# Performance work log

Measured on AMD Instinct MI355X. Metric: run time of the kernel, lower is better.

The kernel has to match this reference:

```python
import jax, jax.numpy as jnp
import numpy as np

N_NODES = 20000
N_EDGES = 320000
IN_F = 256
OUT_F = 64
HEADS = 4
ALPHA = 0.1  # leaky_relu negative slope


def setup_inputs() -> dict:
    key = jax.random.key(0)
    ks = jax.random.split(key, 8)
    return {
        "input1": jax.random.normal(ks[0], (N_NODES, IN_F), jnp.float32),
        "input2": jax.random.normal(ks[1], (N_NODES, IN_F), jnp.float32),
        # per-head params: Ws maps source feats -> target_out, Wt maps target feats -> source_out
        "Ws": jax.random.normal(ks[2], (HEADS, IN_F, OUT_F), jnp.float32) * 0.06,
        "Wt": jax.random.normal(ks[3], (HEADS, IN_F, OUT_F), jnp.float32) * 0.06,
        "a1": jax.random.normal(ks[4], (HEADS, 2 * OUT_F), jnp.float32) * 0.1,
        "a2": jax.random.normal(ks[5], (HEADS, 2 * OUT_F), jnp.float32) * 0.1,
        # COO nonzeros of A_opt [n_target, n_source]
        "tgt_idx": jax.random.randint(ks[6], (N_EDGES,), 0, N_NODES),
        "src_idx": jax.random.randint(ks[7], (N_EDGES,), 0, N_NODES),
    }


def _segment_softmax(scores, seg, num_segments):
    m = jax.lax.stop_gradient(jax.ops.segment_max(scores, seg, num_segments=num_segments))
    w = jnp.exp(scores - m[seg])
    d = jax.ops.segment_sum(w, seg, num_segments=num_segments)
    d = jnp.where(d == 0, 1.0, d)
    return w / d[seg]


def _head(x1, x2, Ws, Wt, a1, a2, src, tgt, n_s, n_t):
    s = x1 @ Ws  # [n_s, OUT_F]  messages source -> target
    t = x2 @ Wt  # [n_t, OUT_F]  messages target -> source
    out = Ws.shape[1]
    # edge score e = leaky_relu(a^T [s_src || t_tgt]); split a to avoid edge-level concat
    e1 = jax.nn.leaky_relu((s @ a1[:out])[src] + (t @ a1[out:])[tgt], ALPHA)
    e2 = jax.nn.leaky_relu((s @ a2[:out])[src] + (t @ a2[out:])[tgt], ALPHA)
    alpha_ts = _segment_softmax(e1, tgt, n_t)  # softmax over sources per target
    alpha_st = _segment_softmax(e2, src, n_s)  # softmax over targets per source
    h_ts = jax.ops.segment_sum(alpha_ts[:, None] * s[src], tgt, num_segments=n_t)
    h_st = jax.ops.segment_sum(alpha_st[:, None] * t[tgt], src, num_segments=n_s)
    return jax.nn.elu(h_st), jax.nn.elu(h_ts)  # concat=True -> ELU per head


def reference(input1, input2, Ws, Wt, a1, a2, tgt_idx, src_idx):
    n_s, n_t = input1.shape[0], input2.shape[0]
    head_fn = jax.vmap(
        lambda W1, W2, v1, v2: _head(input1, input2, W1, W2, v1, v2, src_idx, tgt_idx, n_s, n_t)
    )
    h_st, h_ts = head_fn(Ws, Wt, a1, a2)  # each [H, n, OUT_F]
    h_st = jnp.transpose(h_st, (1, 0, 2)).reshape(n_s, -1)  # concat heads
    h_ts = jnp.transpose(h_ts, (1, 0, 2)).reshape(n_t, -1)
    return h_st, h_ts
```

## Files before the change

### kernel.cpp

```cpp
#include <hip/hip_runtime.h>
#include <math.h>

#define N_NODES 20000
#define N_EDGES 320000
#define IN_F 256
#define OUT_F 64
#define HEADS 4
#define NCOL 256
#define LRELU_ALPHA 0.1f
#define ELL_CAP 64

typedef __attribute__((ext_vector_type(8))) short short8;
typedef __attribute__((ext_vector_type(4))) float floatx4;

__device__ __forceinline__ float lrelu(float x) {
    return x > 0.f ? x : LRELU_ALPHA * x;
}
__device__ __forceinline__ unsigned short f2bf(float f) {
    unsigned int u = __float_as_uint(f);
    u = (u + 0x7FFF + ((u >> 16) & 1)) >> 16;
    return (unsigned short)u;
}
__device__ __forceinline__ float bf2f(unsigned short u) {
    return __uint_as_float(((unsigned int)u) << 16);
}

__global__ __launch_bounds__(256) void prep_build_kernel(
    const int* __restrict__ src, const int* __restrict__ tgt,
    const float* __restrict__ Ws, const float* __restrict__ Wt,
    unsigned short* __restrict__ Wsb, unsigned short* __restrict__ Wtb,
    int* __restrict__ cnt_t, int* __restrict__ cnt_s,
    int* __restrict__ elist_t, int* __restrict__ elist_s)
{
    const int tid = threadIdx.x;
    if (blockIdx.x < 64) {
        const int gid = blockIdx.x * 256 + tid;
        const int mat = gid >> 13;
        const int r   = gid & 8191;
        const int kc  = r >> 8;
        const int c   = r & 255;
        const float* W    = mat ? Wt : Ws;
        unsigned short* O = mat ? Wtb : Wsb;
        const int h = c >> 6, j = c & 63;
        const int k0 = kc * 8;
        unsigned short v[8] __attribute__((aligned(16)));
#pragma unroll
        for (int i = 0; i < 8; ++i)
            v[i] = f2bf(W[(size_t)h * (IN_F * OUT_F) + (size_t)(k0 + i) * OUT_F + j]);
        *(uint4*)(O + (size_t)c * IN_F + k0) = *(const uint4*)v;
    } else {
        const int e = (blockIdx.x - 64) * 256 + tid;
        if (e < N_EDGES) {
            int sn = src[e], tn = tgt[e];
            int p = atomicAdd(&cnt_t[tn], 1);
            if (p < ELL_CAP) elist_t[tn * ELL_CAP + p] = sn;
            int q = atomicAdd(&cnt_s[sn], 1);
            if (q < ELL_CAP) elist_s[sn * ELL_CAP + q] = tn;
        }
    }
}

__global__ __launch_bounds__(256) void gemm_mfma_kernel(
    const float* __restrict__ A0, const unsigned short* __restrict__ Wb0,
    const float* __restrict__ A1, const unsigned short* __restrict__ Wb1,
    unsigned short* __restrict__ C0, unsigned short* __restrict__ C1,
    const float* __restrict__ a1, const float* __restrict__ a2,
    float* __restrict__ ss1, float* __restrict__ ss2,
    float* __restrict__ tt1, float* __restrict__ tt2)
{
    const float* A           = (blockIdx.y == 0) ? A0 : A1;
    const unsigned short* Wb = (blockIdx.y == 0) ? Wb0 : Wb1;
    unsigned short* C        = (blockIdx.y == 0) ? C0 : C1;

    __shared__ __align__(16) unsigned short Bl[256][40];

    const int tid   = threadIdx.x;
    const int lane  = tid & 63;
    const int w     = tid >> 6;
    const int quad  = lane >> 4;
    const int l15   = lane & 15;
    const int mhalf = w & 1, nhalf = w >> 1;
    const int r0    = blockIdx.x * 32;
    const int mrow  = r0 + mhalf * 16 + l15;

    floatx4 acc[8];
#pragma unroll
    for (int t = 0; t < 8; ++t) acc[t] = (floatx4){0.f, 0.f, 0.f, 0.f};

    const float* arow = A + (size_t)mrow * IN_F + quad * 8;

    for (int k0 = 0; k0 < IN_F; k0 += 32) {
#pragma unroll
        for (int p = 0; p < 4; ++p) {
            int idx = p * 256 + tid;
            int n = idx >> 2, kc = idx & 3;
            uint4 v = *(const uint4*)(Wb + (size_t)n * 256 + k0 + kc * 8);
            *(uint4*)&Bl[n][kc * 8] = v;
        }
        __syncthreads();

        float4 av0 = *(const float4*)(arow + k0);
        float4 av1 = *(const float4*)(arow + k0 + 4);
        short8 afrag;
        afrag[0] = (short)f2bf(av0.x); afrag[1] = (short)f2bf(av0.y);
        afrag[2] = (short)f2bf(av0.z); afrag[3] = (short)f2bf(av0.w);
        afrag[4] = (short)f2bf(av1.x); afrag[5] = (short)f2bf(av1.y);
        afrag[6] = (short)f2bf(av1.z); afrag[7] = (short)f2bf(av1.w);

#pragma unroll
        for (int t = 0; t < 8; ++t) {
            int n = (nhalf * 8 + t) * 16 + l15;
            short8 bfrag = *(const short8*)&Bl[n][quad * 8];
            acc[t] = __builtin_amdgcn_mfma_f32_16x16x32_bf16(afrag, bfrag, acc[t], 0, 0, 0);
        }
        __syncthreads();
    }

#pragma unroll
    for (int t = 0; t < 8; ++t) {
        int col = (nhalf * 8 + t) * 16 + l15;
#pragma unroll
        for (int r = 0; r < 4; ++r) {
            int m = r0 + mhalf * 16 + quad * 4 + r;
            C[(size_t)m * NCOL + col] = f2bf(acc[t][r]);
        }
    }

    const int off_aj = (blockIdx.y == 0) ? 0 : 64;
    float* o1 = (blockIdx.y == 0) ? ss1 : tt1;
    float* o2 = (blockIdx.y == 0) ? ss2 : tt2;

    float p1[2][4] = {{0.f,0.f,0.f,0.f},{0.f,0.f,0.f,0.f}};
    float p2[2][4] = {{0.f,0.f,0.f,0.f},{0.f,0.f,0.f,0.f}};
#pragma unroll
    for (int t = 0; t < 8; ++t) {
        int hh = 2 * nhalf + (t >> 2);
        int jj = ((t & 3) * 16) + l15;
        float w1 = a1[hh * 128 + off_aj + jj];
        float w2 = a2[hh * 128 + off_aj + jj];
        int a = t >> 2;
#pragma unroll
        for (int r = 0; r < 4; ++r) {
            p1[a][r] += acc[t][r] * w1;
            p2[a][r] += acc[t][r] * w2;
        }
    }
#pragma unroll
    for (int m = 1; m < 16; m <<= 1) {
#pragma unroll
        for (int a = 0; a < 2; ++a)
#pragma unroll
            for (int r = 0; r < 4; ++r) {
                p1[a][r] += __shfl_xor(p1[a][r], m, 64);
                p2[a][r] += __shfl_xor(p2[a][r], m, 64);
            }
    }
    if (l15 == 0) {
#pragma unroll
        for (int r = 0; r < 4; ++r) {
            int m = r0 + mhalf * 16 + quad * 4 + r;
#pragma unroll
            for (int a = 0; a < 2; ++a) {
                int hh = 2 * nhalf + a;
                o1[m * HEADS + hh] = p1[a][r];
                o2[m * HEADS + hh] = p2[a][r];
            }
        }
    }
}

__global__ __launch_bounds__(256) void agg_kernel(
    const int* __restrict__ cnt_t, const int* __restrict__ elist_t,
    const int* __restrict__ cnt_s, const int* __restrict__ elist_s,
    const float* __restrict__ ss1, const float* __restrict__ ss2,
    const float* __restrict__ tt1, const float* __restrict__ tt2,
    const unsigned short* __restrict__ s_bf, const unsigned short* __restrict__ t_bf,
    float* __restrict__ h_st, float* __restrict__ h_ts)
{
    const int wave = threadIdx.x >> 6;
    const int lane = threadIdx.x & 63;
    const int n    = blockIdx.x * 4 + wave;
    const int dir  = blockIdx.y;
    const int h    = lane >> 4;
    const int coff = lane * 4;

    const int*            cnt   = dir ? cnt_s   : cnt_t;
    const int*            list  = dir ? elist_s : elist_t;
    const unsigned short* table = dir ? t_bf    : s_bf;
    const float*          nsc   = dir ? ss2     : tt1;
    const float*          esc   = dir ? tt2     : ss1;
    float*                outp  = dir ? h_st    : h_ts;

    const float base = nsc[n * HEADS + h];
    int deg = cnt[n];
    if (deg > ELL_CAP) deg = ELL_CAP;
    const int b0 = n * ELL_CAP, b1 = b0 + deg;

    float4 acc = make_float4(0.f, 0.f, 0.f, 0.f);
    float den = 0.f;

    int p = b0;
    for (; p + 1 < b1; p += 2) {
        int m0 = list[p], m1 = list[p + 1];
        float w0 = __expf(lrelu(esc[m0 * HEADS + h] + base));
        float w1 = __expf(lrelu(esc[m1 * HEADS + h] + base));
        ushort4 r0 = *(const ushort4*)(table + (size_t)m0 * NCOL + coff);
        ushort4 r1 = *(const ushort4*)(table + (size_t)m1 * NCOL + coff);
        den += w0 + w1;
        acc.x += w0 * bf2f(r0.x) + w1 * bf2f(r1.x);
        acc.y += w0 * bf2f(r0.y) + w1 * bf2f(r1.y);
        acc.z += w0 * bf2f(r0.z) + w1 * bf2f(r1.z);
        acc.w += w0 * bf2f(r0.w) + w1 * bf2f(r1.w);
    }
    if (p < b1) {
        int m0 = list[p];
        float w0 = __expf(lrelu(esc[m0 * HEADS + h] + base));
        ushort4 r0 = *(const ushort4*)(table + (size_t)m0 * NCOL + coff);
        den += w0;
        acc.x += w0 * bf2f(r0.x);
        acc.y += w0 * bf2f(r0.y);
        acc.z += w0 * bf2f(r0.z);
        acc.w += w0 * bf2f(r0.w);
    }

    if (den == 0.f) den = 1.f;
    float inv = 1.f / den;
    float4 r;
    r.x = acc.x * inv; r.y = acc.y * inv; r.z = acc.z * inv; r.w = acc.w * inv;
    r.x = (r.x > 0.f) ? r.x : expm1f(r.x);
    r.y = (r.y > 0.f) ? r.y : expm1f(r.y);
    r.z = (r.z > 0.f) ? r.z : expm1f(r.z);
    r.w = (r.w > 0.f) ? r.w : expm1f(r.w);
    *(float4*)(outp + (size_t)n * NCOL + coff) = r;
}

extern "C" void kernel_launch(void* const* d_in, const int* in_sizes, int n_in,
                              void* d_out, int out_size, void* d_ws, size_t ws_size,
                              hipStream_t stream)
{
    const float* input1 = (const float*)d_in[0];
    const float* input2 = (const float*)d_in[1];
    const float* Ws     = (const float*)d_in[2];
    const float* Wt     = (const float*)d_in[3];
    const float* a1     = (const float*)d_in[4];
    const float* a2     = (const float*)d_in[5];
    const int*   tgt    = (const int*)d_in[6];
    const int*   src    = (const int*)d_in[7];

    float* out  = (float*)d_out;
    float* h_st = out;
    float* h_ts = out + (size_t)N_NODES * NCOL;

    unsigned short* s_bf = (unsigned short*)d_ws;
    unsigned short* t_bf = s_bf + (size_t)N_NODES * NCOL;
    unsigned short* Wsb  = t_bf + (size_t)N_NODES * NCOL;
    unsigned short* Wtb  = Wsb + 256 * 256;
    float* ss1  = (float*)(Wtb + 256 * 256);
    float* ss2  = ss1 + N_NODES * HEADS;
    float* tt1  = ss2 + N_NODES * HEADS;
    float* tt2  = tt1 + N_NODES * HEADS;
    int*   cnt_t = (int*)(tt2 + N_NODES * HEADS);
    int*   cnt_s = cnt_t + N_NODES;
    int*   elist_t = cnt_s + N_NODES;
    int*   elist_s = elist_t + N_NODES * ELL_CAP;

    hipMemsetAsync(cnt_t, 0, (size_t)2 * N_NODES * sizeof(int), stream);

    prep_build_kernel<<<64 + (N_EDGES + 255) / 256, 256, 0, stream>>>(
        src, tgt, Ws, Wt, Wsb, Wtb, cnt_t, cnt_s, elist_t, elist_s);

    dim3 ggrid(N_NODES / 32, 2);
    gemm_mfma_kernel<<<ggrid, 256, 0, stream>>>(input1, Wsb, input2, Wtb,
                                                s_bf, t_bf, a1, a2,
                                                ss1, ss2, tt1, tt2);

    dim3 agrid(N_NODES / 4, 2);
    agg_kernel<<<agrid, 256, 0, stream>>>(cnt_t, elist_t, cnt_s, elist_s,
                                          ss1, ss2, tt1, tt2, s_bf, t_bf, h_st, h_ts);
}
```

Baseline: 220.8 us.

## Fuse edge-list build into GEMM kernel and fold memset into weight prep

```diff
diff --git a/kernel.cpp b/kernel.cpp
--- a/kernel.cpp
+++ b/kernel.cpp
@@ -25,39 +25,28 @@
     return __uint_as_float(((unsigned int)u) << 16);
 }
 
-__global__ __launch_bounds__(256) void prep_build_kernel(
-    const int* __restrict__ src, const int* __restrict__ tgt,
+__global__ __launch_bounds__(256) void prep_w_kernel(
     const float* __restrict__ Ws, const float* __restrict__ Wt,
     unsigned short* __restrict__ Wsb, unsigned short* __restrict__ Wtb,
-    int* __restrict__ cnt_t, int* __restrict__ cnt_s,
-    int* __restrict__ elist_t, int* __restrict__ elist_s)
-{
-    const int tid = threadIdx.x;
-    if (blockIdx.x < 64) {
-        const int gid = blockIdx.x * 256 + tid;
-        const int mat = gid >> 13;
-        const int r   = gid & 8191;
-        const int kc  = r >> 8;
-        const int c   = r & 255;
-        const float* W    = mat ? Wt : Ws;
-        unsigned short* O = mat ? Wtb : Wsb;
-        const int h = c >> 6, j = c & 63;
-        const int k0 = kc * 8;
-        unsigned short v[8] __attribute__((aligned(16)));
-#pragma unroll
-        for (int i = 0; i < 8; ++i)
-            v[i] = f2bf(W[(size_t)h * (IN_F * OUT_F) + (size_t)(k0 + i) * OUT_F + j]);
-        *(uint4*)(O + (size_t)c * IN_F + k0) = *(const uint4*)v;
-    } else {
-        const int e = (blockIdx.x - 64) * 256 + tid;
-        if (e < N_EDGES) {
-            int sn = src[e], tn = tgt[e];
-            int p = atomicAdd(&cnt_t[tn], 1);
-            if (p < ELL_CAP) elist_t[tn * ELL_CAP + p] = sn;
-            int q = atomicAdd(&cnt_s[sn], 1);
-            if (q < ELL_CAP) elist_s[sn * ELL_CAP + q] = tn;
-        }
-    }
+    int* __restrict__ cnt)
+{
+    const int gid = blockIdx.x * 256 + threadIdx.x;
+
+    for (int i = gid; i < 2 * N_NODES; i += 16384) cnt[i] = 0;
+
+    const int mat = gid >> 13;
+    const int r   = gid & 8191;
+    const int kc  = r >> 8;
+    const int c   = r & 255;
+    const float* W    = mat ? Wt : Ws;
+    unsigned short* O = mat ? Wtb : Wsb;
+    const int h = c >> 6, j = c & 63;
+    const int k0 = kc * 8;
+    unsigned short v[8] __attribute__((aligned(16)));
+#pragma unroll
+    for (int i = 0; i < 8; ++i)
+        v[i] = f2bf(W[(size_t)h * (IN_F * OUT_F) + (size_t)(k0 + i) * OUT_F + j]);
+    *(uint4*)(O + (size_t)c * IN_F + k0) = *(const uint4*)v;
 }
 
 __global__ __launch_bounds__(256) void gemm_mfma_kernel(
@@ -66,15 +55,28 @@
     unsigned short* __restrict__ C0, unsigned short* __restrict__ C1,
     const float* __restrict__ a1, const float* __restrict__ a2,
     float* __restrict__ ss1, float* __restrict__ ss2,
-    float* __restrict__ tt1, float* __restrict__ tt2)
-{
+    float* __restrict__ tt1, float* __restrict__ tt2,
+    const int* __restrict__ src, const int* __restrict__ tgt,
+    int* __restrict__ cnt_t, int* __restrict__ cnt_s,
+    int* __restrict__ elist_t, int* __restrict__ elist_s)
+{
+    const int tid = threadIdx.x;
+
+    {
+        const int e = (blockIdx.y * 625 + blockIdx.x) * 256 + tid;
+        int sn = src[e], tn = tgt[e];
+        int p = atomicAdd(&cnt_t[tn], 1);
+        if (p < ELL_CAP) elist_t[tn * ELL_CAP + p] = sn;
+        int q = atomicAdd(&cnt_s[sn], 1);
+        if (q < ELL_CAP) elist_s[sn * ELL_CAP + q] = tn;
+    }
+
     const float* A           = (blockIdx.y == 0) ? A0 : A1;
     const unsigned short* Wb = (blockIdx.y == 0) ? Wb0 : Wb1;
     unsigned short* C        = (blockIdx.y == 0) ? C0 : C1;
 
     __shared__ __align__(16) unsigned short Bl[256][40];
 
-    const int tid   = threadIdx.x;
     const int lane  = tid & 63;
     const int w     = tid >> 6;
     const int quad  = lane >> 4;
@@ -200,19 +202,26 @@
     float den = 0.f;
 
     int p = b0;
-    for (; p + 1 < b1; p += 2) {
-        int m0 = list[p], m1 = list[p + 1];
-        float w0 = __expf(lrelu(esc[m0 * HEADS + h] + base));
-        float w1 = __expf(lrelu(esc[m1 * HEADS + h] + base));
+    for (; p + 3 < b1; p += 4) {
+        int m0 = list[p],     m1 = list[p + 1];
+        int m2 = list[p + 2], m3 = list[p + 3];
+        float e0 = esc[m0 * HEADS + h], e1 = esc[m1 * HEADS + h];
+        float e2 = esc[m2 * HEADS + h], e3 = esc[m3 * HEADS + h];
         ushort4 r0 = *(const ushort4*)(table + (size_t)m0 * NCOL + coff);
         ushort4 r1 = *(const ushort4*)(table + (size_t)m1 * NCOL + coff);
-        den += w0 + w1;
-        acc.x += w0 * bf2f(r0.x) + w1 * bf2f(r1.x);
-        acc.y += w0 * bf2f(r0.y) + w1 * bf2f(r1.y);
-        acc.z += w0 * bf2f(r0.z) + w1 * bf2f(r1.z);
-        acc.w += w0 * bf2f(r0.w) + w1 * bf2f(r1.w);
-    }
-    if (p < b1) {
+        ushort4 r2 = *(const ushort4*)(table + (size_t)m2 * NCOL + coff);
+        ushort4 r3 = *(const ushort4*)(table + (size_t)m3 * NCOL + coff);
+        float w0 = __expf(lrelu(e0 + base));
+        float w1 = __expf(lrelu(e1 + base));
+        float w2 = __expf(lrelu(e2 + base));
+        float w3 = __expf(lrelu(e3 + base));
+        den += (w0 + w1) + (w2 + w3);
+        acc.x += (w0 * bf2f(r0.x) + w1 * bf2f(r1.x)) + (w2 * bf2f(r2.x) + w3 * bf2f(r3.x));
+        acc.y += (w0 * bf2f(r0.y) + w1 * bf2f(r1.y)) + (w2 * bf2f(r2.y) + w3 * bf2f(r3.y));
+        acc.z += (w0 * bf2f(r0.z) + w1 * bf2f(r1.z)) + (w2 * bf2f(r2.z) + w3 * bf2f(r3.z));
+        acc.w += (w0 * bf2f(r0.w) + w1 * bf2f(r1.w)) + (w2 * bf2f(r2.w) + w3 * bf2f(r3.w));
+    }
+    for (; p < b1; ++p) {
         int m0 = list[p];
         float w0 = __expf(lrelu(esc[m0 * HEADS + h] + base));
         ushort4 r0 = *(const ushort4*)(table + (size_t)m0 * NCOL + coff);
@@ -264,15 +273,14 @@
     int*   elist_t = cnt_s + N_NODES;
     int*   elist_s = elist_t + N_NODES * ELL_CAP;
 
-    hipMemsetAsync(cnt_t, 0, (size_t)2 * N_NODES * sizeof(int), stream);
-
-    prep_build_kernel<<<64 + (N_EDGES + 255) / 256, 256, 0, stream>>>(
-        src, tgt, Ws, Wt, Wsb, Wtb, cnt_t, cnt_s, elist_t, elist_s);
+    prep_w_kernel<<<64, 256, 0, stream>>>(Ws, Wt, Wsb, Wtb, cnt_t);
 
     dim3 ggrid(N_NODES / 32, 2);
     gemm_mfma_kernel<<<ggrid, 256, 0, stream>>>(input1, Wsb, input2, Wtb,
                                                 s_bf, t_bf, a1, a2,
-                                                ss1, ss2, tt1, tt2);
+                                                ss1, ss2, tt1, tt2,
+                                                src, tgt, cnt_t, cnt_s,
+                                                elist_t, elist_s);
 
     dim3 agrid(N_NODES / 4, 2);
     agg_kernel<<<agrid, 256, 0, stream>>>(cnt_t, elist_t, cnt_s, elist_s,
```

New measurement: 203.3 us. 7.9% less time.
